# Performance work log

Measured on AMD Instinct MI355X. Metric: run time of the kernel, lower is better.

The kernel has to match this reference:

```python
import jax, jax.numpy as jnp
import numpy as np

B, N, C, G = 32, 1024, 64, 64

def setup_inputs() -> dict:
    key = jax.random.key(0)
    ks = jax.random.split(key, 8)
    return {
        "x": jax.random.normal(ks[0], (B, N, C), dtype=jnp.float32),
        "valid_len": jax.random.randint(ks[1], (B,), 0, N, dtype=jnp.int64) if jax.config.jax_enable_x64 else jax.random.randint(ks[1], (B,), 0, N, dtype=jnp.int32),
        "Wq": jax.random.normal(ks[2], (C, G), dtype=jnp.float32) * 0.1,
        "bq": jax.random.normal(ks[3], (G,), dtype=jnp.float32) * 0.1,
        "Wk": jax.random.normal(ks[4], (C, G), dtype=jnp.float32) * 0.1,
        "bk": jax.random.normal(ks[5], (G,), dtype=jnp.float32) * 0.1,
        "Wv": jax.random.normal(ks[6], (C, G), dtype=jnp.float32) * 0.1,
        "bv": jax.random.normal(ks[7], (G,), dtype=jnp.float32) * 0.1,
    }

def reference(x, valid_len, Wq, bq, Wk, bk, Wv, bv):
    # x: [B, N, C]; valid_len: [B] int (number of valid key positions per batch)
    q = x @ Wq + bq                                   # [B, N, G]
    k = x @ Wk + bk                                   # [B, N, G]
    v = x @ Wv + bv                                   # [B, N, G]
    scores = jnp.einsum('bnd,bmd->bnm', q, k)         # [B, N, N] (no 1/sqrt(d) scale)
    # mask: key positions >= valid_len[b] get -1e6 (matches original's -1000000.0 fill)
    col = jnp.arange(scores.shape[-1])
    mask = col[None, None, :] >= valid_len[:, None, None]
    scores = jnp.where(mask, jnp.float32(-1000000.0), scores)
    attn = jax.nn.softmax(scores, axis=-1)            # [B, N, N]
    return jnp.einsum('bnm,bmd->bnd', attn, v)        # [B, N, G]
```

## Files before the change

### kernel.cpp

```cpp
#include <hip/hip_runtime.h>
#include <stdint.h>


typedef __attribute__((ext_vector_type(4))) float    floatx4;
typedef __attribute__((ext_vector_type(8))) _Float16 halfx8;

static __device__ __forceinline__ unsigned short f2h(float f) {
    union { _Float16 h; unsigned short u; } v; v.h = (_Float16)f;
    return v.u;
}
static __device__ __forceinline__ float h2f(unsigned short u) {
    union { unsigned short u; _Float16 h; } v; v.u = u;
    return (float)v.h;
}

#define MFMA16(a, bb, c) __builtin_amdgcn_mfma_f32_16x16x32_f16((a), (bb), (c), 0, 0, 0)

__global__ __launch_bounds__(256, 2) void proj_kernel(
    const float* __restrict__ x,
    const float* __restrict__ Wq, const float* __restrict__ bq,
    const float* __restrict__ Wk, const float* __restrict__ bk,
    const float* __restrict__ Wv, const float* __restrict__ bv,
    unsigned short* __restrict__ qimg,
    unsigned short* __restrict__ kimg,
    unsigned short* __restrict__ vimg)
{
    __shared__ __align__(16) unsigned short sm[24576];
    const int XH = 0, XL = 4096, WQH = 8192, WQL = 12288, WKH = 16384, WVH = 20480;

    const int tid  = threadIdx.x;
    const int blk  = blockIdx.x;
    const int lane = tid & 63;
    const int w    = tid >> 6;
    const int l15  = lane & 15;
    const int quad = lane >> 4;
    const int rl   = lane >> 2;
    const int c8a  = 2 * (lane & 3);
    const int c8b  = c8a + 1;
    const int sidx_a = rl * 64 + ((c8a ^ (rl & 7)) * 8);
    const int sidx_b = rl * 64 + ((c8b ^ (rl & 7)) * 8);

    {
        const float* xrow = x + (size_t)(blk * 64 + w * 16) * 64;
#pragma unroll
        for (int i = 0; i < 2; ++i) {
            int c8   = (i == 0) ? c8a : c8b;
            int sidx = (i == 0) ? sidx_a : sidx_b;
            const float4* gp = (const float4*)(xrow + rl * 64 + c8 * 8);
            float4 f0 = gp[0], f1 = gp[1];
            float fv[8] = { f0.x, f0.y, f0.z, f0.w, f1.x, f1.y, f1.z, f1.w };
            __align__(16) unsigned short thi[8], tlo[8];
#pragma unroll
            for (int j = 0; j < 8; ++j) {
                unsigned short hi = f2h(fv[j]);
                thi[j] = hi;
                tlo[j] = f2h(fv[j] - h2f(hi));
            }
            *(uint4*)&sm[XH + w * 1024 + sidx] = *(uint4*)thi;
            *(uint4*)&sm[XL + w * 1024 + sidx] = *(uint4*)tlo;
        }
    }
    {
        int g = tid & 63, ci = tid >> 6;
#pragma unroll
        for (int j = 0; j < 16; ++j) {
            int c = ci * 16 + j;
            int idx = g * 64 + (((c >> 3) ^ (g & 7)) * 8) + (c & 7);
            float fq = Wq[c * 64 + g];
            unsigned short qhi = f2h(fq);
            sm[WQH + idx] = qhi;
            sm[WQL + idx] = f2h(fq - h2f(qhi));
            sm[WKH + idx] = f2h(Wk[c * 64 + g]);
            sm[WVH + idx] = f2h(Wv[c * 64 + g]);
        }
    }
    __syncthreads();

    const int fidx0 = l15 * 64 + (((0 + quad) ^ (l15 & 7)) * 8);
    const int fidx1 = l15 * 64 + (((4 + quad) ^ (l15 & 7)) * 8);
    halfx8 ah0 = *(const halfx8*)&sm[XH + w * 1024 + fidx0];
    halfx8 ah1 = *(const halfx8*)&sm[XH + w * 1024 + fidx1];
    halfx8 al0 = *(const halfx8*)&sm[XL + w * 1024 + fidx0];
    halfx8 al1 = *(const halfx8*)&sm[XL + w * 1024 + fidx1];

    floatx4 vacc[4];
#pragma unroll
    for (int gs = 0; gs < 4; ++gs) {
        int brow = gs * 16 + l15;
        int b0 = brow * 64 + (((0 + quad) ^ (brow & 7)) * 8);
        int b1 = brow * 64 + (((4 + quad) ^ (brow & 7)) * 8);
        halfx8 bh0 = *(const halfx8*)&sm[WQH + b0];
        halfx8 bh1 = *(const halfx8*)&sm[WQH + b1];
        halfx8 bl0 = *(const halfx8*)&sm[WQL + b0];
        halfx8 bl1 = *(const halfx8*)&sm[WQL + b1];
        halfx8 wk0 = *(const halfx8*)&sm[WKH + b0];
        halfx8 wk1 = *(const halfx8*)&sm[WKH + b1];
        halfx8 wv0 = *(const halfx8*)&sm[WVH + b0];
        halfx8 wv1 = *(const halfx8*)&sm[WVH + b1];

        float bbq = bq[gs * 16 + l15];
        floatx4 qa = { bbq, bbq, bbq, bbq };
        qa = MFMA16(ah0, bh0, qa);
        qa = MFMA16(ah1, bh1, qa);
        qa = MFMA16(ah0, bl0, qa);
        qa = MFMA16(ah1, bl1, qa);
        qa = MFMA16(al0, bh0, qa);
        qa = MFMA16(al1, bh1, qa);

        float bbk = bk[gs * 16 + l15];
        float bbv = bv[gs * 16 + l15];
        floatx4 ka = { bbk, bbk, bbk, bbk };
        floatx4 va = { bbv, bbv, bbv, bbv };
        ka = MFMA16(ah0, wk0, ka);
        ka = MFMA16(ah1, wk1, ka);
        va = MFMA16(ah0, wv0, va);
        va = MFMA16(ah1, wv1, va);
        vacc[gs] = va;

        int c8 = gs * 2 + (l15 >> 3);
#pragma unroll
        for (int r = 0; r < 4; ++r) {
            int row = w * 16 + quad * 4 + r;
            int idx = row * 64 + ((c8 ^ (row & 7)) * 8) + (l15 & 7);
            sm[XH + idx] = f2h(qa[r]);
            sm[XL + idx] = f2h(ka[r]);
        }
    }
    __syncthreads();
#pragma unroll
    for (int gs = 0; gs < 4; ++gs) {
        int g = gs * 16 + l15;
#pragma unroll
        for (int r = 0; r < 4; ++r) {
            int key = w * 16 + quad * 4 + r;
            sm[WQH + g * 64 + (((key >> 3) ^ (g & 7)) * 8) + (key & 7)] = f2h(vacc[gs][r]);
        }
    }
    __syncthreads();

    {
        const size_t tb = (size_t)blk * 4096;
#pragma unroll
        for (int i = 0; i < 2; ++i) {
            int ci = i * 256 + tid;
            *(uint4*)&qimg[tb + ci * 8] = *(const uint4*)&sm[XH  + ci * 8];
            *(uint4*)&kimg[tb + ci * 8] = *(const uint4*)&sm[XL  + ci * 8];
            *(uint4*)&vimg[tb + ci * 8] = *(const uint4*)&sm[WQH + ci * 8];
        }
    }
}

__global__ __launch_bounds__(256, 2) void attn_kernel(
    const unsigned short* __restrict__ qimg,
    const unsigned short* __restrict__ kimg,
    const unsigned short* __restrict__ vimg,
    const int* __restrict__ valid_len, float* __restrict__ out)
{
    __shared__ __align__(16) unsigned short psmem[4096];
    __shared__ int sched[32];

    const int tid  = threadIdx.x;
    const int blk  = blockIdx.x;
    const int lane = tid & 63;
    const int w    = tid >> 6;
    const int l15  = lane & 15;
    const int quad = lane >> 4;

    if (tid < 32) {
        int vlb = valid_len[tid];
        int ntb = (vlb == 0) ? 16 : ((vlb + 63) >> 6);
        int rank = 0;
        for (int b2 = 0; b2 < 32; ++b2) {
            int vl2 = valid_len[b2];
            int nt2 = (vl2 == 0) ? 16 : ((vl2 + 63) >> 6);
            rank += (nt2 > ntb) || (nt2 == ntb && b2 < tid);
        }
        sched[rank] = tid;
    }
    __syncthreads();

    const int b    = (blk < 256) ? sched[blk >> 4] : sched[31 - ((blk - 256) >> 4)];
    const int qt   = blk & 15;
    const int row0 = b * 1024 + qt * 64;

    const int vl    = valid_len[b];
    const int nt    = (vl == 0) ? 16 : ((vl + 63) >> 6);
    const int fullt = vl >> 6;

    const int arow = w * 16 + l15;
    const unsigned short* qb = qimg + (size_t)(b * 16 + qt) * 4096;
    halfx8 aq0 = *(const halfx8*)&qb[arow * 64 + (((0 + quad) ^ (arow & 7)) * 8)];
    halfx8 aq1 = *(const halfx8*)&qb[arow * 64 + (((4 + quad) ^ (arow & 7)) * 8)];

    int idx0[4], idx1[4];
#pragma unroll
    for (int sub = 0; sub < 4; ++sub) {
        int r = sub * 16 + l15;
        idx0[sub] = r * 64 + (((0 + quad) ^ (r & 7)) * 8);
        idx1[sub] = r * 64 + (((4 + quad) ^ (r & 7)) * 8);
    }

    const unsigned short* kt_base = kimg + (size_t)b * 65536;
    const unsigned short* vt_base = vimg + (size_t)b * 65536;

    float m_r[4]    = { -INFINITY, -INFINITY, -INFINITY, -INFINITY };
    float l_lane[4] = { 0.f, 0.f, 0.f, 0.f };
    floatx4 o[4] = { {0,0,0,0}, {0,0,0,0}, {0,0,0,0}, {0,0,0,0} };

    unsigned short* psw = &psmem[w * 1024];

    halfx8 kf0[4], kf1[4];
#pragma unroll
    for (int sub = 0; sub < 4; ++sub) {
        kf0[sub] = *(const halfx8*)&kt_base[idx0[sub]];
        kf1[sub] = *(const halfx8*)&kt_base[idx1[sub]];
    }

    for (int t = 0; t < nt; ++t) {
        const unsigned short* vt = vt_base + (size_t)t * 4096;
        halfx8 vf0[4], vf1[4];
#pragma unroll
        for (int sub = 0; sub < 4; ++sub) {
            vf0[sub] = *(const halfx8*)&vt[idx0[sub]];
            vf1[sub] = *(const halfx8*)&vt[idx1[sub]];
        }

        floatx4 s[4];
#pragma unroll
        for (int sub = 0; sub < 4; ++sub) {
            floatx4 acc = { 0, 0, 0, 0 };
            acc = MFMA16(aq0, kf0[sub], acc);
            acc = MFMA16(aq1, kf1[sub], acc);
            s[sub] = acc;
        }

        const bool pre = (t + 1) < nt;
        halfx8 nk0[4], nk1[4];
        if (pre) {
            const unsigned short* ktn = kt_base + (size_t)(t + 1) * 4096;
#pragma unroll
            for (int sub = 0; sub < 4; ++sub) {
                nk0[sub] = *(const halfx8*)&ktn[idx0[sub]];
                nk1[sub] = *(const halfx8*)&ktn[idx1[sub]];
            }
        }

        if (t >= fullt) {
#pragma unroll
            for (int sub = 0; sub < 4; ++sub) {
                int key = t * 64 + sub * 16 + l15;
                if (key >= vl) { s[sub][0] = -1e6f; s[sub][1] = -1e6f; s[sub][2] = -1e6f; s[sub][3] = -1e6f; }
            }
        }

        float p[4][4];
        float alpha[4];
#pragma unroll
        for (int r = 0; r < 4; ++r) {
            float mx = fmaxf(fmaxf(s[0][r], s[1][r]), fmaxf(s[2][r], s[3][r]));
#pragma unroll
            for (int off = 1; off < 16; off <<= 1)
                mx = fmaxf(mx, __shfl_xor(mx, off, 64));
            float mnew = fmaxf(m_r[r], mx);
            alpha[r] = __expf(m_r[r] - mnew);
            float psum = 0.f;
#pragma unroll
            for (int sub = 0; sub < 4; ++sub) {
                float pv = __expf(s[sub][r] - mnew);
                p[sub][r] = pv;
                psum += pv;
            }
            l_lane[r] = l_lane[r] * alpha[r] + psum;
            m_r[r] = mnew;
        }
#pragma unroll
        for (int gs = 0; gs < 4; ++gs) {
            o[gs][0] *= alpha[0]; o[gs][1] *= alpha[1];
            o[gs][2] *= alpha[2]; o[gs][3] *= alpha[3];
        }

#pragma unroll
        for (int sub = 0; sub < 4; ++sub) {
            int c8 = sub * 2 + (l15 >> 3);
#pragma unroll
            for (int r = 0; r < 4; ++r) {
                int row = quad * 4 + r;
                psw[row * 64 + ((c8 ^ (row & 7)) * 8) + (l15 & 7)] = f2h(p[sub][r]);
            }
        }
        halfx8 ap0 = *(const halfx8*)&psw[l15 * 64 + (((0 + quad) ^ (l15 & 7)) * 8)];
        halfx8 ap1 = *(const halfx8*)&psw[l15 * 64 + (((4 + quad) ^ (l15 & 7)) * 8)];

#pragma unroll
        for (int gs = 0; gs < 4; ++gs) {
            o[gs] = MFMA16(ap0, vf0[gs], o[gs]);
            o[gs] = MFMA16(ap1, vf1[gs], o[gs]);
        }

        if (pre) {
#pragma unroll
            for (int sub = 0; sub < 4; ++sub) {
                kf0[sub] = nk0[sub];
                kf1[sub] = nk1[sub];
            }
        }
    }

    float l[4];
#pragma unroll
    for (int r = 0; r < 4; ++r) {
        float ss = l_lane[r];
#pragma unroll
        for (int off = 1; off < 16; off <<= 1)
            ss += __shfl_xor(ss, off, 64);
        l[r] = ss;
    }
#pragma unroll
    for (int gs = 0; gs < 4; ++gs) {
#pragma unroll
        for (int r = 0; r < 4; ++r) {
            int row = row0 + w * 16 + quad * 4 + r;
            out[row * 64 + gs * 16 + l15] = o[gs][r] / l[r];
        }
    }
}

__global__ __launch_bounds__(256, 2) void fused_attn_fallback(
    const float* __restrict__ x,
    const float* __restrict__ Wq, const float* __restrict__ bq,
    const float* __restrict__ Wk, const float* __restrict__ bk,
    const float* __restrict__ Wv, const float* __restrict__ bv,
    const int* __restrict__ valid_len, float* __restrict__ out)
{
    __shared__ __align__(16) unsigned short smem[28672];
    __shared__ int sched[32];

    const int Q_OFF = 0, XH_OFF = 4096, KL0_OFF = 8192, KL1_OFF = 12288,
              VS0_OFF = 16384, VS1_OFF = 20480, PS_OFF = 24576;

    const int tid  = threadIdx.x;
    const int blk  = blockIdx.x;
    const int lane = tid & 63;
    const int w    = tid >> 6;
    const int l15  = lane & 15;
    const int quad = lane >> 4;

    if (tid < 32) {
        int vlb = valid_len[tid];
        int ntb = (vlb == 0) ? 16 : ((vlb + 63) >> 6);
        int rank = 0;
        for (int b2 = 0; b2 < 32; ++b2) {
            int vl2 = valid_len[b2];
            int nt2 = (vl2 == 0) ? 16 : ((vl2 + 63) >> 6);
            rank += (nt2 > ntb) || (nt2 == ntb && b2 < tid);
        }
        sched[rank] = tid;
    }
    __syncthreads();

    const int hv   = (blk < 256);
    const int b    = hv ? sched[blk >> 4] : sched[31 - ((blk - 256) >> 4)];
    const int n0   = (blk & 15) * 64;
    const int row0 = b * 1024 + n0;

    const int xsl  = XH_OFF + w * 1024;
    const int fidx0 = l15 * 64 + (((0 + quad) ^ (l15 & 7)) * 8);
    const int fidx1 = l15 * 64 + (((4 + quad) ^ (l15 & 7)) * 8);
    const int rl   = lane >> 2;
    const int c8a  = 2 * (lane & 3);
    const int c8b  = 2 * (lane & 3) + 1;
    const int sidx_a = rl * 64 + ((c8a ^ (rl & 7)) * 8);
    const int sidx_b = rl * 64 + ((c8b ^ (rl & 7)) * 8);

    const int vl    = valid_len[b];
    const int nt    = (vl == 0) ? 16 : ((vl + 63) >> 6);
    const int fullt = vl >> 6;

    {
        const float* xrow = x + (size_t)(row0 + w * 16) * 64;
#pragma unroll
        for (int i = 0; i < 2; ++i) {
            int c8 = (i == 0) ? c8a : c8b;
            int sidx = (i == 0) ? sidx_a : sidx_b;
            const float4* gp = (const float4*)(xrow + rl * 64 + c8 * 8);
            float4 f0 = gp[0], f1 = gp[1];
            float fv[8] = { f0.x, f0.y, f0.z, f0.w, f1.x, f1.y, f1.z, f1.w };
            __align__(16) unsigned short thi[8], tlo[8];
#pragma unroll
            for (int j = 0; j < 8; ++j) {
                unsigned short hi = f2h(fv[j]);
                thi[j] = hi;
                tlo[j] = f2h(fv[j] - h2f(hi));
            }
            *(uint4*)&smem[xsl + sidx]                = *(uint4*)thi;
            *(uint4*)&smem[VS0_OFF + w * 1024 + sidx] = *(uint4*)tlo;
        }
    }
    {
        int g = tid & 63, ci = tid >> 6;
#pragma unroll
        for (int j = 0; j < 16; ++j) {
            int c = ci * 16 + j;
            int idx = g * 64 + (((c >> 3) ^ (g & 7)) * 8) + (c & 7);
            float fq = Wq[c * 64 + g];
            unsigned short qhi = f2h(fq);
            smem[KL0_OFF + idx] = qhi;
            smem[KL1_OFF + idx] = f2h(fq - h2f(qhi));
            smem[VS1_OFF + idx] = f2h(Wk[c * 64 + g]);
            smem[PS_OFF  + idx] = f2h(Wv[c * 64 + g]);
        }
    }
    __syncthreads();

    halfx8 wkf0[4], wkf1[4], wvf0[4], wvf1[4];
#pragma unroll
    for (int gs = 0; gs < 4; ++gs) {
        int brow = gs * 16 + l15;
        int b0 = brow * 64 + (((0 + quad) ^ (brow & 7)) * 8);
        int b1 = brow * 64 + (((4 + quad) ^ (brow & 7)) * 8);
        wkf0[gs] = *(const halfx8*)&smem[VS1_OFF + b0];
        wkf1[gs] = *(const halfx8*)&smem[VS1_OFF + b1];
        wvf0[gs] = *(const halfx8*)&smem[PS_OFF + b0];
        wvf1[gs] = *(const halfx8*)&smem[PS_OFF + b1];
    }

    {
        halfx8 ah0 = *(const halfx8*)&smem[xsl + fidx0];
        halfx8 ah1 = *(const halfx8*)&smem[xsl + fidx1];
        halfx8 al0 = *(const halfx8*)&smem[VS0_OFF + w * 1024 + fidx0];
        halfx8 al1 = *(const halfx8*)&smem[VS0_OFF + w * 1024 + fidx1];
#pragma unroll
        for (int gs = 0; gs < 4; ++gs) {
            int brow = gs * 16 + l15;
            float bb = bq[gs * 16 + l15];
            floatx4 acc = { bb, bb, bb, bb };
            int b0 = brow * 64 + (((0 + quad) ^ (brow & 7)) * 8);
            int b1 = brow * 64 + (((4 + quad) ^ (brow & 7)) * 8);
            halfx8 bh0 = *(const halfx8*)&smem[KL0_OFF + b0];
            halfx8 bh1 = *(const halfx8*)&smem[KL0_OFF + b1];
            halfx8 bl0 = *(const halfx8*)&smem[KL1_OFF + b0];
            halfx8 bl1 = *(const halfx8*)&smem[KL1_OFF + b1];
            acc = MFMA16(ah0, bh0, acc);
            acc = MFMA16(ah1, bh1, acc);
            acc = MFMA16(ah0, bl0, acc);
            acc = MFMA16(ah1, bl1, acc);
            acc = MFMA16(al0, bh0, acc);
            acc = MFMA16(al1, bh1, acc);
            int c8 = gs * 2 + (l15 >> 3);
#pragma unroll
            for (int r = 0; r < 4; ++r) {
                int row = w * 16 + quad * 4 + r;
                smem[Q_OFF + row * 64 + ((c8 ^ (row & 7)) * 8) + (l15 & 7)] = f2h(acc[r]);
            }
        }
    }
    const int arow = w * 16 + l15;
    halfx8 aq0 = *(const halfx8*)&smem[Q_OFF + arow * 64 + (((0 + quad) ^ (arow & 7)) * 8)];
    halfx8 aq1 = *(const halfx8*)&smem[Q_OFF + arow * 64 + (((4 + quad) ^ (arow & 7)) * 8)];

    {
        const float* xrow = x + (size_t)(b * 1024 + w * 16) * 64;
#pragma unroll
        for (int i = 0; i < 2; ++i) {
            int c8 = (i == 0) ? c8a : c8b;
            int sidx = (i == 0) ? sidx_a : sidx_b;
            const float4* gp = (const float4*)(xrow + rl * 64 + c8 * 8);
            float4 f0 = gp[0], f1 = gp[1];
            __align__(16) unsigned short thi[8] = {
                f2h(f0.x), f2h(f0.y), f2h(f0.z), f2h(f0.w),
                f2h(f1.x), f2h(f1.y), f2h(f1.z), f2h(f1.w) };
            *(uint4*)&smem[xsl + sidx] = *(uint4*)thi;
        }
    }
    __syncthreads();

    {
        halfx8 kxh0 = *(const halfx8*)&smem[xsl + fidx0];
        halfx8 kxh1 = *(const halfx8*)&smem[xsl + fidx1];
#pragma unroll
        for (int gs = 0; gs < 4; ++gs) {
            float bbk = bk[gs * 16 + l15];
            float bbv = bv[gs * 16 + l15];
            floatx4 kacc = { bbk, bbk, bbk, bbk };
            floatx4 vacc = { bbv, bbv, bbv, bbv };
            kacc = MFMA16(kxh0, wkf0[gs], kacc);
            kacc = MFMA16(kxh1, wkf1[gs], kacc);
            vacc = MFMA16(kxh0, wvf0[gs], vacc);
            vacc = MFMA16(kxh1, wvf1[gs], vacc);
            int c8 = gs * 2 + (l15 >> 3);
            int g  = gs * 16 + l15;
#pragma unroll
            for (int r = 0; r < 4; ++r) {
                int key = w * 16 + quad * 4 + r;
                smem[KL0_OFF + key * 64 + ((c8 ^ (key & 7)) * 8) + (l15 & 7)] = f2h(kacc[r]);
                smem[VS0_OFF + g * 64 + (((key >> 3) ^ (g & 7)) * 8) + (key & 7)] = f2h(vacc[r]);
            }
        }
    }

    float m_r[4]    = { -INFINITY, -INFINITY, -INFINITY, -INFINITY };
    float l_lane[4] = { 0.f, 0.f, 0.f, 0.f };
    floatx4 o[4] = { {0,0,0,0}, {0,0,0,0}, {0,0,0,0}, {0,0,0,0} };

    for (int t = 0; t < nt; ++t) {
        bool pre = (t + 1) < nt;
        float4 pfa0, pfa1, pfb0, pfb1;
        if (pre) {
            const float* xrow = x + (size_t)(b * 1024 + (t + 1) * 64 + w * 16) * 64;
            pfa0 = ((const float4*)(xrow + rl * 64 + c8a * 8))[0];
            pfa1 = ((const float4*)(xrow + rl * 64 + c8a * 8))[1];
            pfb0 = ((const float4*)(xrow + rl * 64 + c8b * 8))[0];
            pfb1 = ((const float4*)(xrow + rl * 64 + c8b * 8))[1];
        }
        __syncthreads();

        if (pre) {
            __align__(16) unsigned short ta[8] = {
                f2h(pfa0.x), f2h(pfa0.y), f2h(pfa0.z), f2h(pfa0.w),
                f2h(pfa1.x), f2h(pfa1.y), f2h(pfa1.z), f2h(pfa1.w) };
            __align__(16) unsigned short tb[8] = {
                f2h(pfb0.x), f2h(pfb0.y), f2h(pfb0.z), f2h(pfb0.w),
                f2h(pfb1.x), f2h(pfb1.y), f2h(pfb1.z), f2h(pfb1.w) };
            *(uint4*)&smem[xsl + sidx_a] = *(uint4*)ta;
            *(uint4*)&smem[xsl + sidx_b] = *(uint4*)tb;
            halfx8 kxh0 = *(const halfx8*)&smem[xsl + fidx0];
            halfx8 kxh1 = *(const halfx8*)&smem[xsl + fidx1];
            const int KLn = ((t + 1) & 1) ? KL1_OFF : KL0_OFF;
            const int VSn = ((t + 1) & 1) ? VS1_OFF : VS0_OFF;
#pragma unroll
            for (int gs = 0; gs < 4; ++gs) {
                float bbk = bk[gs * 16 + l15];
                float bbv = bv[gs * 16 + l15];
                floatx4 kacc = { bbk, bbk, bbk, bbk };
                floatx4 vacc = { bbv, bbv, bbv, bbv };
                kacc = MFMA16(kxh0, wkf0[gs], kacc);
                kacc = MFMA16(kxh1, wkf1[gs], kacc);
                vacc = MFMA16(kxh0, wvf0[gs], vacc);
                vacc = MFMA16(kxh1, wvf1[gs], vacc);
                int c8 = gs * 2 + (l15 >> 3);
                int g  = gs * 16 + l15;
#pragma unroll
                for (int r = 0; r < 4; ++r) {
                    int key = w * 16 + quad * 4 + r;
                    smem[KLn + key * 64 + ((c8 ^ (key & 7)) * 8) + (l15 & 7)] = f2h(kacc[r]);
                    smem[VSn + g * 64 + (((key >> 3) ^ (g & 7)) * 8) + (key & 7)] = f2h(vacc[r]);
                }
            }
        }

        const int KLc = (t & 1) ? KL1_OFF : KL0_OFF;
        const int VSc = (t & 1) ? VS1_OFF : VS0_OFF;

        floatx4 s[4];
#pragma unroll
        for (int sub = 0; sub < 4; ++sub) {
            int krow = sub * 16 + l15;
            halfx8 bk0 = *(const halfx8*)&smem[KLc + krow * 64 + (((0 + quad) ^ (krow & 7)) * 8)];
            halfx8 bk1 = *(const halfx8*)&smem[KLc + krow * 64 + (((4 + quad) ^ (krow & 7)) * 8)];
            floatx4 acc = { 0, 0, 0, 0 };
            acc = MFMA16(aq0, bk0, acc);
            acc = MFMA16(aq1, bk1, acc);
            s[sub] = acc;
        }
        if (t >= fullt) {
#pragma unroll
            for (int sub = 0; sub < 4; ++sub) {
                int key = t * 64 + sub * 16 + l15;
                if (key >= vl) { s[sub][0] = -1e6f; s[sub][1] = -1e6f; s[sub][2] = -1e6f; s[sub][3] = -1e6f; }
            }
        }

        float p[4][4];
        float alpha[4];
#pragma unroll
        for (int r = 0; r < 4; ++r) {
            float mx = fmaxf(fmaxf(s[0][r], s[1][r]), fmaxf(s[2][r], s[3][r]));
#pragma unroll
            for (int off = 1; off < 16; off <<= 1)
                mx = fmaxf(mx, __shfl_xor(mx, off, 64));
            float mnew = fmaxf(m_r[r], mx);
            alpha[r] = __expf(m_r[r] - mnew);
            float psum = 0.f;
#pragma unroll
            for (int sub = 0; sub < 4; ++sub) {
                float pv = __expf(s[sub][r] - mnew);
                p[sub][r] = pv;
                psum += pv;
            }
            l_lane[r] = l_lane[r] * alpha[r] + psum;
            m_r[r] = mnew;
        }
#pragma unroll
        for (int gs = 0; gs < 4; ++gs) {
            o[gs][0] *= alpha[0]; o[gs][1] *= alpha[1];
            o[gs][2] *= alpha[2]; o[gs][3] *= alpha[3];
        }

        unsigned short* psw = &smem[PS_OFF + w * 1024];
#pragma unroll
        for (int sub = 0; sub < 4; ++sub) {
            int c8 = sub * 2 + (l15 >> 3);
#pragma unroll
            for (int r = 0; r < 4; ++r) {
                int row = quad * 4 + r;
                psw[row * 64 + ((c8 ^ (row & 7)) * 8) + (l15 & 7)] = f2h(p[sub][r]);
            }
        }
        halfx8 ap0 = *(const halfx8*)&psw[fidx0];
        halfx8 ap1 = *(const halfx8*)&psw[fidx1];

#pragma unroll
        for (int gs = 0; gs < 4; ++gs) {
            int grow = gs * 16 + l15;
            halfx8 bv0 = *(const halfx8*)&smem[VSc + grow * 64 + (((0 + quad) ^ (grow & 7)) * 8)];
            halfx8 bv1 = *(const halfx8*)&smem[VSc + grow * 64 + (((4 + quad) ^ (grow & 7)) * 8)];
            o[gs] = MFMA16(ap0, bv0, o[gs]);
            o[gs] = MFMA16(ap1, bv1, o[gs]);
        }
    }

    float l[4];
#pragma unroll
    for (int r = 0; r < 4; ++r) {
        float ss = l_lane[r];
#pragma unroll
        for (int off = 1; off < 16; off <<= 1)
            ss += __shfl_xor(ss, off, 64);
        l[r] = ss;
    }
#pragma unroll
    for (int gs = 0; gs < 4; ++gs) {
#pragma unroll
        for (int r = 0; r < 4; ++r) {
            int row = row0 + w * 16 + quad * 4 + r;
            out[row * 64 + gs * 16 + l15] = o[gs][r] / l[r];
        }
    }
}

extern "C" void kernel_launch(void* const* d_in, const int* in_sizes, int n_in,
                              void* d_out, int out_size, void* d_ws, size_t ws_size,
                              hipStream_t stream) {
    const float* x    = (const float*)d_in[0];
    const int*   vlen = (const int*)  d_in[1];
    const float* Wq   = (const float*)d_in[2];
    const float* bq   = (const float*)d_in[3];
    const float* Wk   = (const float*)d_in[4];
    const float* bk   = (const float*)d_in[5];
    const float* Wv   = (const float*)d_in[6];
    const float* bv   = (const float*)d_in[7];
    float* out = (float*)d_out;

    const size_t IMG_SHORTS = (size_t)32 * 16 * 4096;
    const size_t NEED = 3 * IMG_SHORTS * sizeof(unsigned short);

    if (ws_size >= NEED) {
        unsigned short* qimg = (unsigned short*)d_ws;
        unsigned short* kimg = qimg + IMG_SHORTS;
        unsigned short* vimg = kimg + IMG_SHORTS;
        proj_kernel<<<512, 256, 0, stream>>>(x, Wq, bq, Wk, bk, Wv, bv,
                                             qimg, kimg, vimg);
        attn_kernel<<<512, 256, 0, stream>>>(qimg, kimg, vimg, vlen, out);
    } else {
        fused_attn_fallback<<<512, 256, 0, stream>>>(
            x, Wq, bq, Wk, bk, Wv, bv, vlen, out);
    }
}
```

Measured before the change: 99.11 us.

## Prefetch V tiles one step ahead and remap blocks to batches across XCDs

The attention loop now double-buffers V fragments along with K, loading tile t+1's K and V before the QK MFMAs, so V load latency is hidden behind compute. Block-to-batch mapping changes to rank_of_blk, which interleaves work by blk&7 (likely XCD round-robin) to balance long and short batches across XCDs. The projection kernel uses the same mapping so each XCD's L2 may already hold the K/V images it wrote. This costs more registers per thread, and the projection kernel now also computes the schedule.

```diff
diff --git a/kernel.cpp b/kernel.cpp
--- a/kernel.cpp
+++ b/kernel.cpp
@@ -16,16 +16,24 @@
 
 #define MFMA16(a, bb, c) __builtin_amdgcn_mfma_f32_16x16x32_f16((a), (bb), (c), 0, 0, 0)
 
+static __device__ __forceinline__ int rank_of_blk(int blk) {
+    int x = blk & 7;
+    int s = blk >> 7;
+    return (s == 0) ? x : (s == 1) ? 15 - x : (s == 2) ? 31 - x : 16 + x;
+}
+
 __global__ __launch_bounds__(256, 2) void proj_kernel(
     const float* __restrict__ x,
     const float* __restrict__ Wq, const float* __restrict__ bq,
     const float* __restrict__ Wk, const float* __restrict__ bk,
     const float* __restrict__ Wv, const float* __restrict__ bv,
+    const int* __restrict__ valid_len,
     unsigned short* __restrict__ qimg,
     unsigned short* __restrict__ kimg,
     unsigned short* __restrict__ vimg)
 {
     __shared__ __align__(16) unsigned short sm[24576];
+    __shared__ int sched[32];
     const int XH = 0, XL = 4096, WQH = 8192, WQL = 12288, WKH = 16384, WVH = 20480;
 
     const int tid  = threadIdx.x;
@@ -40,8 +48,25 @@
     const int sidx_a = rl * 64 + ((c8a ^ (rl & 7)) * 8);
     const int sidx_b = rl * 64 + ((c8b ^ (rl & 7)) * 8);
 
-    {
-        const float* xrow = x + (size_t)(blk * 64 + w * 16) * 64;
+    if (tid < 32) {
+        int vlb = valid_len[tid];
+        int ntb = (vlb == 0) ? 16 : ((vlb + 63) >> 6);
+        int rank = 0;
+        for (int b2 = 0; b2 < 32; ++b2) {
+            int vl2 = valid_len[b2];
+            int nt2 = (vl2 == 0) ? 16 : ((vl2 + 63) >> 6);
+            rank += (nt2 > ntb) || (nt2 == ntb && b2 < tid);
+        }
+        sched[rank] = tid;
+    }
+    __syncthreads();
+
+    const int b  = sched[rank_of_blk(blk)];
+    const int qt = (blk >> 3) & 15;
+    const int tile = b * 16 + qt;
+
+    {
+        const float* xrow = x + (size_t)(tile * 64 + w * 16) * 64;
 #pragma unroll
         for (int i = 0; i < 2; ++i) {
             int c8   = (i == 0) ? c8a : c8b;
@@ -139,7 +164,7 @@
     __syncthreads();
 
     {
-        const size_t tb = (size_t)blk * 4096;
+        const size_t tb = (size_t)tile * 4096;
 #pragma unroll
         for (int i = 0; i < 2; ++i) {
             int ci = i * 256 + tid;
@@ -179,8 +204,8 @@
     }
     __syncthreads();
 
-    const int b    = (blk < 256) ? sched[blk >> 4] : sched[31 - ((blk - 256) >> 4)];
-    const int qt   = blk & 15;
+    const int b    = sched[rank_of_blk(blk)];
+    const int qt   = (blk >> 3) & 15;
     const int row0 = b * 1024 + qt * 64;
 
     const int vl    = valid_len[b];
@@ -209,20 +234,28 @@
 
     unsigned short* psw = &psmem[w * 1024];
 
-    halfx8 kf0[4], kf1[4];
+    halfx8 kf0[4], kf1[4], vf0[4], vf1[4];
 #pragma unroll
     for (int sub = 0; sub < 4; ++sub) {
         kf0[sub] = *(const halfx8*)&kt_base[idx0[sub]];
         kf1[sub] = *(const halfx8*)&kt_base[idx1[sub]];
+        vf0[sub] = *(const halfx8*)&vt_base[idx0[sub]];
+        vf1[sub] = *(const halfx8*)&vt_base[idx1[sub]];
     }
 
     for (int t = 0; t < nt; ++t) {
-        const unsigned short* vt = vt_base + (size_t)t * 4096;
-        halfx8 vf0[4], vf1[4];
-#pragma unroll
-        for (int sub = 0; sub < 4; ++sub) {
-            vf0[sub] = *(const halfx8*)&vt[idx0[sub]];
-            vf1[sub] = *(const halfx8*)&vt[idx1[sub]];
+        const bool pre = (t + 1) < nt;
+        halfx8 nk0[4], nk1[4], nv0[4], nv1[4];
+        if (pre) {
+            const unsigned short* ktn = kt_base + (size_t)(t + 1) * 4096;
+            const unsigned short* vtn = vt_base + (size_t)(t + 1) * 4096;
+#pragma unroll
+            for (int sub = 0; sub < 4; ++sub) {
+                nk0[sub] = *(const halfx8*)&ktn[idx0[sub]];
+                nk1[sub] = *(const halfx8*)&ktn[idx1[sub]];
+                nv0[sub] = *(const halfx8*)&vtn[idx0[sub]];
+                nv1[sub] = *(const halfx8*)&vtn[idx1[sub]];
+            }
         }
 
         floatx4 s[4];
@@ -234,17 +267,6 @@
             s[sub] = acc;
         }
 
-        const bool pre = (t + 1) < nt;
-        halfx8 nk0[4], nk1[4];
-        if (pre) {
-            const unsigned short* ktn = kt_base + (size_t)(t + 1) * 4096;
-#pragma unroll
-            for (int sub = 0; sub < 4; ++sub) {
-                nk0[sub] = *(const halfx8*)&ktn[idx0[sub]];
-                nk1[sub] = *(const halfx8*)&ktn[idx1[sub]];
-            }
-        }
-
         if (t >= fullt) {
 #pragma unroll
             for (int sub = 0; sub < 4; ++sub) {
@@ -302,6 +324,8 @@
             for (int sub = 0; sub < 4; ++sub) {
                 kf0[sub] = nk0[sub];
                 kf1[sub] = nk1[sub];
+                vf0[sub] = nv0[sub];
+                vf1[sub] = nv1[sub];
             }
         }
     }
@@ -658,7 +682,7 @@
         unsigned short* qimg = (unsigned short*)d_ws;
         unsigned short* kimg = qimg + IMG_SHORTS;
         unsigned short* vimg = kimg + IMG_SHORTS;
-        proj_kernel<<<512, 256, 0, stream>>>(x, Wq, bq, Wk, bk, Wv, bv,
+        proj_kernel<<<512, 256, 0, stream>>>(x, Wq, bq, Wk, bk, Wv, bv, vlen,
                                              qimg, kimg, vimg);
         attn_kernel<<<512, 256, 0, stream>>>(qimg, kimg, vimg, vlen, out);
     } else {
```

Result: slower. 105.6 us (+6.5%).

## Software-pipeline attention loop: defer PV matmul one tile, double-buffer P and V

Applied to the files above, without the earlier changes.

Restructures the flash-attention inner loop so the P·V MFMA for tile t-1 runs while tile t's QK scores and softmax are computed. The P tile now lives in a double-buffered LDS region and V fragments in two register sets, with a prefetch of the next V tile issued mid-iteration. The goal is to hide global-load and LDS latency behind MFMA work and cut serial dependencies. In exchange it doubles shared memory for P and adds register pressure, which may affect occupancy at launch_bounds(256,2).

```diff
diff --git a/kernel.cpp b/kernel.cpp
--- a/kernel.cpp
+++ b/kernel.cpp
@@ -156,7 +156,7 @@
     const unsigned short* __restrict__ vimg,
     const int* __restrict__ valid_len, float* __restrict__ out)
 {
-    __shared__ __align__(16) unsigned short psmem[4096];
+    __shared__ __align__(16) unsigned short psmem[8192];
     __shared__ int sched[32];
 
     const int tid  = threadIdx.x;
@@ -199,110 +199,205 @@
         idx0[sub] = r * 64 + (((0 + quad) ^ (r & 7)) * 8);
         idx1[sub] = r * 64 + (((4 + quad) ^ (r & 7)) * 8);
     }
+    const int fpidx0 = l15 * 64 + (((0 + quad) ^ (l15 & 7)) * 8);
+    const int fpidx1 = l15 * 64 + (((4 + quad) ^ (l15 & 7)) * 8);
 
     const unsigned short* kt_base = kimg + (size_t)b * 65536;
     const unsigned short* vt_base = vimg + (size_t)b * 65536;
 
     float m_r[4]    = { -INFINITY, -INFINITY, -INFINITY, -INFINITY };
     float l_lane[4] = { 0.f, 0.f, 0.f, 0.f };
+    float aprev[4]  = { 0.f, 0.f, 0.f, 0.f };
     floatx4 o[4] = { {0,0,0,0}, {0,0,0,0}, {0,0,0,0}, {0,0,0,0} };
 
-    unsigned short* psw = &psmem[w * 1024];
+    unsigned short* psw0 = &psmem[w * 1024];
+    unsigned short* psw1 = &psmem[4096 + w * 1024];
 
     halfx8 kf0[4], kf1[4];
+    halfx8 vfA0[4], vfA1[4], vfB0[4], vfB1[4];
 #pragma unroll
     for (int sub = 0; sub < 4; ++sub) {
-        kf0[sub] = *(const halfx8*)&kt_base[idx0[sub]];
-        kf1[sub] = *(const halfx8*)&kt_base[idx1[sub]];
-    }
-
-    for (int t = 0; t < nt; ++t) {
-        const unsigned short* vt = vt_base + (size_t)t * 4096;
-        halfx8 vf0[4], vf1[4];
-#pragma unroll
-        for (int sub = 0; sub < 4; ++sub) {
-            vf0[sub] = *(const halfx8*)&vt[idx0[sub]];
-            vf1[sub] = *(const halfx8*)&vt[idx1[sub]];
-        }
-
-        floatx4 s[4];
+        kf0[sub]  = *(const halfx8*)&kt_base[idx0[sub]];
+        kf1[sub]  = *(const halfx8*)&kt_base[idx1[sub]];
+        vfA0[sub] = *(const halfx8*)&vt_base[idx0[sub]];
+        vfA1[sub] = *(const halfx8*)&vt_base[idx1[sub]];
+    }
+
+#define TILE_BODY(T, VS0, VS1, PW, PR)                                         \
+    {                                                                          \
+        floatx4 s_[4];                                                         \
+        _Pragma("unroll")                                                      \
+        for (int sub = 0; sub < 4; ++sub) {                                    \
+            floatx4 acc = { 0, 0, 0, 0 };                                      \
+            acc = MFMA16(aq0, kf0[sub], acc);                                  \
+            acc = MFMA16(aq1, kf1[sub], acc);                                  \
+            s_[sub] = acc;                                                     \
+        }                                                                      \
+        if ((T) + 1 < nt) {         \
+            const unsigned short* ktn = kt_base + (size_t)((T) + 1) * 4096;    \
+            _Pragma("unroll")                                                  \
+            for (int sub = 0; sub < 4; ++sub) {                                \
+                kf0[sub] = *(const halfx8*)&ktn[idx0[sub]];                    \
+                kf1[sub] = *(const halfx8*)&ktn[idx1[sub]];                    \
+            }                                                                  \
+        }                                                                      \
+        if ((T) >= fullt) {                                                    \
+            _Pragma("unroll")                                                  \
+            for (int sub = 0; sub < 4; ++sub) {                                \
+                int key = (T) * 64 + sub * 16 + l15;                           \
+                if (key >= vl) { s_[sub][0] = -1e6f; s_[sub][1] = -1e6f;       \
+                                 s_[sub][2] = -1e6f; s_[sub][3] = -1e6f; }     \
+            }                                                                  \
+        }                                                                      \
+        float p_[4][4];                                                        \
+        float alpha_[4];                                                       \
+        _Pragma("unroll")                                                      \
+        for (int r = 0; r < 4; ++r) {                                          \
+            float mx = fmaxf(fmaxf(s_[0][r], s_[1][r]),                        \
+                             fmaxf(s_[2][r], s_[3][r]));                       \
+            _Pragma("unroll")                                                  \
+            for (int off = 1; off < 16; off <<= 1)                             \
+                mx = fmaxf(mx, __shfl_xor(mx, off, 64));                       \
+            float mnew = fmaxf(m_r[r], mx);                                    \
+            alpha_[r] = __expf(m_r[r] - mnew);                                 \
+            float psum = 0.f;                                                  \
+            _Pragma("unroll")                                                  \
+            for (int sub = 0; sub < 4; ++sub) {                                \
+                float pv = __expf(s_[sub][r] - mnew);                          \
+                p_[sub][r] = pv;                                               \
+                psum += pv;                                                    \
+            }                                                                  \
+            l_lane[r] = l_lane[r] * alpha_[r] + psum;                          \
+            m_r[r] = mnew;                                                     \
+        }                                                                      \
+        {               \
+            halfx8 ap0 = *(const halfx8*)&(PR)[fpidx0];                        \
+            halfx8 ap1 = *(const halfx8*)&(PR)[fpidx1];                        \
+            _Pragma("unroll")                                                  \
+            for (int gs = 0; gs < 4; ++gs) {                                   \
+                o[gs][0] *= aprev[0]; o[gs][1] *= aprev[1];                    \
+                o[gs][2] *= aprev[2]; o[gs][3] *= aprev[3];                    \
+                o[gs] = MFMA16(ap0, VS0[gs], o[gs]);                           \
+                o[gs] = MFMA16(ap1, VS1[gs], o[gs]);                           \
+            }                                                                  \
+        }                                                                      \
+        if ((T) + 1 < nt) {          \
+            const unsigned short* vtn = vt_base + (size_t)((T) + 1) * 4096;    \
+            _Pragma("unroll")                                                  \
+            for (int sub = 0; sub < 4; ++sub) {                                \
+                VS0[sub] = *(const halfx8*)&vtn[idx0[sub]];                    \
+                VS1[sub] = *(const halfx8*)&vtn[idx1[sub]];                    \
+            }                                                                  \
+        }                                                                      \
+        _Pragma("unroll")                                      \
+        for (int sub = 0; sub < 4; ++sub) {                                    \
+            int c8 = sub * 2 + (l15 >> 3);                                     \
+            _Pragma("unroll")                                                  \
+            for (int r = 0; r < 4; ++r) {                                      \
+                int row = quad * 4 + r;                                        \
+                (PW)[row * 64 + ((c8 ^ (row & 7)) * 8) + (l15 & 7)] =          \
+                    f2h(p_[sub][r]);                                           \
+            }                                                                  \
+        }                                                                      \
+        aprev[0] = alpha_[0]; aprev[1] = alpha_[1];                            \
+        aprev[2] = alpha_[2]; aprev[3] = alpha_[3];                            \
+    }
+
+    {
+        floatx4 s_[4];
 #pragma unroll
         for (int sub = 0; sub < 4; ++sub) {
             floatx4 acc = { 0, 0, 0, 0 };
             acc = MFMA16(aq0, kf0[sub], acc);
             acc = MFMA16(aq1, kf1[sub], acc);
-            s[sub] = acc;
-        }
-
-        const bool pre = (t + 1) < nt;
-        halfx8 nk0[4], nk1[4];
-        if (pre) {
-            const unsigned short* ktn = kt_base + (size_t)(t + 1) * 4096;
+            s_[sub] = acc;
+        }
+        if (nt > 1) {
+            const unsigned short* ktn = kt_base + 4096;
 #pragma unroll
             for (int sub = 0; sub < 4; ++sub) {
-                nk0[sub] = *(const halfx8*)&ktn[idx0[sub]];
-                nk1[sub] = *(const halfx8*)&ktn[idx1[sub]];
-            }
-        }
-
-        if (t >= fullt) {
+                kf0[sub] = *(const halfx8*)&ktn[idx0[sub]];
+                kf1[sub] = *(const halfx8*)&ktn[idx1[sub]];
+            }
+        }
+        if (0 >= fullt) {
 #pragma unroll
             for (int sub = 0; sub < 4; ++sub) {
-                int key = t * 64 + sub * 16 + l15;
-                if (key >= vl) { s[sub][0] = -1e6f; s[sub][1] = -1e6f; s[sub][2] = -1e6f; s[sub][3] = -1e6f; }
-            }
-        }
-
-        float p[4][4];
-        float alpha[4];
+                int key = sub * 16 + l15;
+                if (key >= vl) { s_[sub][0] = -1e6f; s_[sub][1] = -1e6f;
+                                 s_[sub][2] = -1e6f; s_[sub][3] = -1e6f; }
+            }
+        }
+        float p_[4][4];
+        float alpha_[4];
 #pragma unroll
         for (int r = 0; r < 4; ++r) {
-            float mx = fmaxf(fmaxf(s[0][r], s[1][r]), fmaxf(s[2][r], s[3][r]));
+            float mx = fmaxf(fmaxf(s_[0][r], s_[1][r]), fmaxf(s_[2][r], s_[3][r]));
 #pragma unroll
             for (int off = 1; off < 16; off <<= 1)
                 mx = fmaxf(mx, __shfl_xor(mx, off, 64));
             float mnew = fmaxf(m_r[r], mx);
-            alpha[r] = __expf(m_r[r] - mnew);
+            alpha_[r] = __expf(m_r[r] - mnew);
             float psum = 0.f;
 #pragma unroll
             for (int sub = 0; sub < 4; ++sub) {
-                float pv = __expf(s[sub][r] - mnew);
-                p[sub][r] = pv;
+                float pv = __expf(s_[sub][r] - mnew);
+                p_[sub][r] = pv;
                 psum += pv;
             }
-            l_lane[r] = l_lane[r] * alpha[r] + psum;
+            l_lane[r] = l_lane[r] * alpha_[r] + psum;
             m_r[r] = mnew;
         }
-#pragma unroll
-        for (int gs = 0; gs < 4; ++gs) {
-            o[gs][0] *= alpha[0]; o[gs][1] *= alpha[1];
-            o[gs][2] *= alpha[2]; o[gs][3] *= alpha[3];
-        }
-
+        if (nt > 1) {
+            const unsigned short* vtn = vt_base + 4096;
+#pragma unroll
+            for (int sub = 0; sub < 4; ++sub) {
+                vfB0[sub] = *(const halfx8*)&vtn[idx0[sub]];
+                vfB1[sub] = *(const halfx8*)&vtn[idx1[sub]];
+            }
+        }
 #pragma unroll
         for (int sub = 0; sub < 4; ++sub) {
             int c8 = sub * 2 + (l15 >> 3);
 #pragma unroll
             for (int r = 0; r < 4; ++r) {
                 int row = quad * 4 + r;
-                psw[row * 64 + ((c8 ^ (row & 7)) * 8) + (l15 & 7)] = f2h(p[sub][r]);
-            }
-        }
-        halfx8 ap0 = *(const halfx8*)&psw[l15 * 64 + (((0 + quad) ^ (l15 & 7)) * 8)];
-        halfx8 ap1 = *(const halfx8*)&psw[l15 * 64 + (((4 + quad) ^ (l15 & 7)) * 8)];
-
+                psw0[row * 64 + ((c8 ^ (row & 7)) * 8) + (l15 & 7)] = f2h(p_[sub][r]);
+            }
+        }
+        aprev[0] = alpha_[0]; aprev[1] = alpha_[1];
+        aprev[2] = alpha_[2]; aprev[3] = alpha_[3];
+    }
+
+    int t = 1;
+    for (; t + 1 < nt; t += 2) {
+        TILE_BODY(t,     vfA0, vfA1, psw1, psw0);
+        TILE_BODY(t + 1, vfB0, vfB1, psw0, psw1);
+    }
+    if (t < nt) {
+        TILE_BODY(t, vfA0, vfA1, psw1, psw0);
+    }
+#undef TILE_BODY
+
+    if (((nt - 1) & 1) == 0) {
+        halfx8 ap0 = *(const halfx8*)&psw0[fpidx0];
+        halfx8 ap1 = *(const halfx8*)&psw0[fpidx1];
 #pragma unroll
         for (int gs = 0; gs < 4; ++gs) {
-            o[gs] = MFMA16(ap0, vf0[gs], o[gs]);
-            o[gs] = MFMA16(ap1, vf1[gs], o[gs]);
-        }
-
-        if (pre) {
-#pragma unroll
-            for (int sub = 0; sub < 4; ++sub) {
-                kf0[sub] = nk0[sub];
-                kf1[sub] = nk1[sub];
-            }
+            o[gs][0] *= aprev[0]; o[gs][1] *= aprev[1];
+            o[gs][2] *= aprev[2]; o[gs][3] *= aprev[3];
+            o[gs] = MFMA16(ap0, vfA0[gs], o[gs]);
+            o[gs] = MFMA16(ap1, vfA1[gs], o[gs]);
+        }
+    } else {
+        halfx8 ap0 = *(const halfx8*)&psw1[fpidx0];
+        halfx8 ap1 = *(const halfx8*)&psw1[fpidx1];
+#pragma unroll
+        for (int gs = 0; gs < 4; ++gs) {
+            o[gs][0] *= aprev[0]; o[gs][1] *= aprev[1];
+            o[gs][2] *= aprev[2]; o[gs][3] *= aprev[3];
+            o[gs] = MFMA16(ap0, vfB0[gs], o[gs]);
+            o[gs] = MFMA16(ap1, vfB1[gs], o[gs]);
         }
     }
 
```

Result: faster. 97.05 us (-2.1%).

## Split attention key range across two blocks and merge partial softmax results

Applied to the files above, without the earlier changes.

The attention kernel now runs 1024 blocks. Each query tile's key tiles are split into two halves, and each half writes an unnormalised partial output plus its running max and sum to workspace. A new merge kernel rescales and combines the two partials into the final output. This aims to shorten the critical path set by batches with long valid lengths and to raise parallelism on the GPU. The K/V prefetch is also reorganised to load the next V tile after the PV MFMAs, and occupancy is raised to 3 blocks per SM. The cost is an extra kernel launch, a larger workspace requirement, and round-tripping about 16MB of fp32 partials through global memory.

```diff
diff --git a/kernel.cpp b/kernel.cpp
--- a/kernel.cpp
+++ b/kernel.cpp
@@ -150,11 +150,12 @@
     }
 }
 
-__global__ __launch_bounds__(256, 2) void attn_kernel(
+__global__ __launch_bounds__(256, 3) void attn_split_kernel(
     const unsigned short* __restrict__ qimg,
     const unsigned short* __restrict__ kimg,
     const unsigned short* __restrict__ vimg,
-    const int* __restrict__ valid_len, float* __restrict__ out)
+    const int* __restrict__ valid_len,
+    float* __restrict__ po, float* __restrict__ pml)
 {
     __shared__ __align__(16) unsigned short psmem[4096];
     __shared__ int sched[32];
@@ -179,16 +180,43 @@
     }
     __syncthreads();
 
-    const int b    = (blk < 256) ? sched[blk >> 4] : sched[31 - ((blk - 256) >> 4)];
-    const int qt   = blk & 15;
-    const int row0 = b * 1024 + qt * 64;
+    const int half = blk >> 9;
+    const int idx  = blk & 511;
+    const int b    = (idx < 256) ? sched[idx >> 4] : sched[31 - ((idx - 256) >> 4)];
+    const int qt   = idx & 15;
+    const int tb   = b * 16 + qt;
 
     const int vl    = valid_len[b];
     const int nt    = (vl == 0) ? 16 : ((vl + 63) >> 6);
     const int fullt = vl >> 6;
+    const int ht    = (nt + 1) >> 1;
+    const int t0    = half ? ht : 0;
+    const int t1    = half ? nt : ht;
+
+    float* pob  = po  + (size_t)(half * 512 + tb) * 4096;
+    float* pmlb = pml + (size_t)(half * 512 + tb) * 128;
+
+    if (t0 >= t1) {
+#pragma unroll
+        for (int gs = 0; gs < 4; ++gs)
+#pragma unroll
+            for (int r = 0; r < 4; ++r) {
+                int qr = w * 16 + quad * 4 + r;
+                pob[qr * 64 + gs * 16 + l15] = 0.f;
+            }
+        if (l15 == 0) {
+#pragma unroll
+            for (int r = 0; r < 4; ++r) {
+                int qr = w * 16 + quad * 4 + r;
+                pmlb[qr * 2 + 0] = -INFINITY;
+                pmlb[qr * 2 + 1] = 0.f;
+            }
+        }
+        return;
+    }
 
     const int arow = w * 16 + l15;
-    const unsigned short* qb = qimg + (size_t)(b * 16 + qt) * 4096;
+    const unsigned short* qb = qimg + (size_t)tb * 4096;
     halfx8 aq0 = *(const halfx8*)&qb[arow * 64 + (((0 + quad) ^ (arow & 7)) * 8)];
     halfx8 aq1 = *(const halfx8*)&qb[arow * 64 + (((4 + quad) ^ (arow & 7)) * 8)];
 
@@ -199,6 +227,8 @@
         idx0[sub] = r * 64 + (((0 + quad) ^ (r & 7)) * 8);
         idx1[sub] = r * 64 + (((4 + quad) ^ (r & 7)) * 8);
     }
+    const int fpidx0 = l15 * 64 + (((0 + quad) ^ (l15 & 7)) * 8);
+    const int fpidx1 = l15 * 64 + (((4 + quad) ^ (l15 & 7)) * 8);
 
     const unsigned short* kt_base = kimg + (size_t)b * 65536;
     const unsigned short* vt_base = vimg + (size_t)b * 65536;
@@ -209,22 +239,20 @@
 
     unsigned short* psw = &psmem[w * 1024];
 
-    halfx8 kf0[4], kf1[4];
-#pragma unroll
-    for (int sub = 0; sub < 4; ++sub) {
-        kf0[sub] = *(const halfx8*)&kt_base[idx0[sub]];
-        kf1[sub] = *(const halfx8*)&kt_base[idx1[sub]];
-    }
-
-    for (int t = 0; t < nt; ++t) {
-        const unsigned short* vt = vt_base + (size_t)t * 4096;
-        halfx8 vf0[4], vf1[4];
+    halfx8 kf0[4], kf1[4], vf0[4], vf1[4];
+    {
+        const unsigned short* kt = kt_base + (size_t)t0 * 4096;
+        const unsigned short* vt = vt_base + (size_t)t0 * 4096;
 #pragma unroll
         for (int sub = 0; sub < 4; ++sub) {
+            kf0[sub] = *(const halfx8*)&kt[idx0[sub]];
+            kf1[sub] = *(const halfx8*)&kt[idx1[sub]];
             vf0[sub] = *(const halfx8*)&vt[idx0[sub]];
             vf1[sub] = *(const halfx8*)&vt[idx1[sub]];
         }
-
+    }
+
+    for (int t = t0; t < t1; ++t) {
         floatx4 s[4];
 #pragma unroll
         for (int sub = 0; sub < 4; ++sub) {
@@ -234,14 +262,13 @@
             s[sub] = acc;
         }
 
-        const bool pre = (t + 1) < nt;
-        halfx8 nk0[4], nk1[4];
+        const bool pre = (t + 1) < t1;
         if (pre) {
             const unsigned short* ktn = kt_base + (size_t)(t + 1) * 4096;
 #pragma unroll
             for (int sub = 0; sub < 4; ++sub) {
-                nk0[sub] = *(const halfx8*)&ktn[idx0[sub]];
-                nk1[sub] = *(const halfx8*)&ktn[idx1[sub]];
+                kf0[sub] = *(const halfx8*)&ktn[idx0[sub]];
+                kf1[sub] = *(const halfx8*)&ktn[idx1[sub]];
             }
         }
 
@@ -288,8 +315,8 @@
                 psw[row * 64 + ((c8 ^ (row & 7)) * 8) + (l15 & 7)] = f2h(p[sub][r]);
             }
         }
-        halfx8 ap0 = *(const halfx8*)&psw[l15 * 64 + (((0 + quad) ^ (l15 & 7)) * 8)];
-        halfx8 ap1 = *(const halfx8*)&psw[l15 * 64 + (((4 + quad) ^ (l15 & 7)) * 8)];
+        halfx8 ap0 = *(const halfx8*)&psw[fpidx0];
+        halfx8 ap1 = *(const halfx8*)&psw[fpidx1];
 
 #pragma unroll
         for (int gs = 0; gs < 4; ++gs) {
@@ -298,10 +325,11 @@
         }
 
         if (pre) {
+            const unsigned short* vtn = vt_base + (size_t)(t + 1) * 4096;
 #pragma unroll
             for (int sub = 0; sub < 4; ++sub) {
-                kf0[sub] = nk0[sub];
-                kf1[sub] = nk1[sub];
+                vf0[sub] = *(const halfx8*)&vtn[idx0[sub]];
+                vf1[sub] = *(const halfx8*)&vtn[idx1[sub]];
             }
         }
     }
@@ -319,9 +347,53 @@
     for (int gs = 0; gs < 4; ++gs) {
 #pragma unroll
         for (int r = 0; r < 4; ++r) {
-            int row = row0 + w * 16 + quad * 4 + r;
-            out[row * 64 + gs * 16 + l15] = o[gs][r] / l[r];
-        }
+            int qr = w * 16 + quad * 4 + r;
+            pob[qr * 64 + gs * 16 + l15] = o[gs][r];
+        }
+    }
+    if (l15 == 0) {
+#pragma unroll
+        for (int r = 0; r < 4; ++r) {
+            int qr = w * 16 + quad * 4 + r;
+            pmlb[qr * 2 + 0] = m_r[r];
+            pmlb[qr * 2 + 1] = l[r];
+        }
+    }
+}
+
+__global__ __launch_bounds__(256, 4) void merge_kernel(
+    const float* __restrict__ po, const float* __restrict__ pml,
+    float* __restrict__ out)
+{
+    const int bk  = blockIdx.x;
+    const int tid = threadIdx.x;
+    const int r   = tid >> 2;
+    const int g0  = (tid & 3) * 16;
+
+    float m1 = pml[(size_t)bk * 128 + r * 2];
+    float l1 = pml[(size_t)bk * 128 + r * 2 + 1];
+    float m2 = pml[(size_t)(512 + bk) * 128 + r * 2];
+    float l2 = pml[(size_t)(512 + bk) * 128 + r * 2 + 1];
+    float m  = fmaxf(m1, m2);
+    float w1 = __expf(m1 - m);
+    float w2 = __expf(m2 - m);
+    float L  = l1 * w1 + l2 * w2;
+
+    const float* p1 = po + (size_t)bk * 4096 + r * 64 + g0;
+    const float* p2 = po + (size_t)(512 + bk) * 4096 + r * 64 + g0;
+    const int b = bk >> 4, qt = bk & 15;
+    float* op = out + (size_t)(b * 1024 + qt * 64 + r) * 64 + g0;
+
+#pragma unroll
+    for (int j = 0; j < 16; j += 4) {
+        float4 a = *(const float4*)(p1 + j);
+        float4 c = *(const float4*)(p2 + j);
+        float4 d;
+        d.x = (a.x * w1 + c.x * w2) / L;
+        d.y = (a.y * w1 + c.y * w2) / L;
+        d.z = (a.z * w1 + c.z * w2) / L;
+        d.w = (a.w * w1 + c.w * w2) / L;
+        *(float4*)(op + j) = d;
     }
 }
 
@@ -652,15 +724,22 @@
     float* out = (float*)d_out;
 
     const size_t IMG_SHORTS = (size_t)32 * 16 * 4096;
-    const size_t NEED = 3 * IMG_SHORTS * sizeof(unsigned short);
+    const size_t PO_FLOATS  = (size_t)2 * 512 * 4096;
+    const size_t PML_FLOATS = (size_t)2 * 512 * 128;
+    const size_t NEED = 3 * IMG_SHORTS * sizeof(unsigned short)
+                      + (PO_FLOATS + PML_FLOATS) * sizeof(float);
 
     if (ws_size >= NEED) {
         unsigned short* qimg = (unsigned short*)d_ws;
         unsigned short* kimg = qimg + IMG_SHORTS;
         unsigned short* vimg = kimg + IMG_SHORTS;
+        float* po  = (float*)(vimg + IMG_SHORTS);
+        float* pml = po + PO_FLOATS;
         proj_kernel<<<512, 256, 0, stream>>>(x, Wq, bq, Wk, bk, Wv, bv,
                                              qimg, kimg, vimg);
-        attn_kernel<<<512, 256, 0, stream>>>(qimg, kimg, vimg, vlen, out);
+        attn_split_kernel<<<1024, 256, 0, stream>>>(qimg, kimg, vimg, vlen,
+                                                    po, pml);
+        merge_kernel<<<512, 256, 0, stream>>>(po, pml, out);
     } else {
         fused_attn_fallback<<<512, 256, 0, stream>>>(
             x, Wq, bq, Wk, bk, Wv, bv, vlen, out);
```

Result: slower. 112.8 us (+13.8%).
